# Optimization experiments

Hardware: AMD Instinct MI355X
Metric: run time of the kernel (lower is better)

The kernel has to match this reference:

```python
import jax, jax.numpy as jnp
import numpy as np

EPS = 1e-8  # torch cosine_similarity eps


def setup_inputs() -> dict:
    key = jax.random.key(0)
    ks = jax.random.split(key, 6)
    N, D, E, mask_dim = 50000, 128, 600000, 1
    x = jax.random.normal(ks[0], (N, D), dtype=jnp.float32)
    mask = jax.random.normal(ks[1], (N, mask_dim), dtype=jnp.float32)
    edge_index = jax.random.randint(ks[2], (2, E), 0, N, dtype=jnp.int64)
    # Linear(input_dim, input_dim) params (orthogonal-ish init not needed for math check)
    W = jax.random.normal(ks[3], (D, D), dtype=jnp.float32) / np.sqrt(D)
    b_lin = jax.random.normal(ks[4], (D,), dtype=jnp.float32) * 0.01
    alpha = jnp.float32(0.001)
    bias = jnp.ones((mask_dim,), dtype=jnp.float32) * -3.0
    return {"x": x, "mask": mask, "edge_index": edge_index,
            "W": W, "b_lin": b_lin, "alpha": alpha, "bias": bias}


def _forward(x, mask, W, b_lin, alpha, bias, edge_index, K=5):
    N = x.shape[0]
    # x_fn: Linear + Tanh
    h = jnp.tanh(x @ W.T + b_lin)                    # [N, D]
    row, col = edge_index[0], edge_index[1]
    hs, hd = h[row], h[col]                          # [E, D] gathers
    ns = jnp.maximum(jnp.linalg.norm(hs, axis=-1), EPS)
    nd = jnp.maximum(jnp.linalg.norm(hd, axis=-1), EPS)
    cos = jnp.sum(hs * hd, axis=-1) / (ns * nd)      # [E]
    edge_weights = jax.nn.relu(cos)

    # APPNP with PyG defaults: gcn_norm with self-loops (weight 1), sym norm
    loops = jnp.arange(N, dtype=row.dtype)
    r2 = jnp.concatenate([row, loops])
    c2 = jnp.concatenate([col, loops])
    w2 = jnp.concatenate([edge_weights, jnp.ones((N,), dtype=edge_weights.dtype)])
    deg = jax.ops.segment_sum(w2, c2, num_segments=N)
    dinv = jnp.where(deg > 0, deg ** -0.5, 0.0)
    norm = dinv[r2] * w2 * dinv[c2]                  # [E+N]

    h0 = jax.nn.relu(mask)                           # [N, 1]
    f = h0
    for _ in range(K):
        msg = norm[:, None] * f[r2]                  # gather + weight
        agg = jax.ops.segment_sum(msg, c2, num_segments=N)  # scatter-add to targets
        f = (1.0 - alpha) * agg + alpha * h0
    fill = jnp.tanh(f - jax.nn.softplus(bias))
    return fill, edge_weights


def reference(x, mask, edge_index, W, b_lin, alpha, bias):
    return _forward(x, mask, W, b_lin, alpha, bias, edge_index, K=5)
```

## Files before the change

### kernel.cpp

```cpp
#include <hip/hip_runtime.h>
#include <hip/hip_bf16.h>
#include <hip/hip_fp16.h>
#include <math.h>

typedef _Float16 half8 __attribute__((ext_vector_type(8)));
typedef float f32x4 __attribute__((ext_vector_type(4)));

__device__ __forceinline__ float tanh_fast(float v) {
  float e = __expf(v + v);
  return 1.0f - 2.0f * __builtin_amdgcn_rcpf(e + 1.0f);
}

__device__ __forceinline__ float dot8h(float4 a, float4 b) {
  const __half2* pa = (const __half2*)&a;
  const __half2* pb = (const __half2*)&b;
  float s = 0.0f;
#pragma unroll
  for (int i = 0; i < 4; ++i) {
    float2 fa = __half22float2(pa[i]);
    float2 fb = __half22float2(pb[i]);
    s = fmaf(fa.x, fb.x, s);
    s = fmaf(fa.y, fb.y, s);
  }
  return s;
}

__global__ __launch_bounds__(256) void k_front(
    const float* __restrict__ x, const float* __restrict__ W,
    const float* __restrict__ bl, const float* __restrict__ mask,
    const int* __restrict__ cols, __half* __restrict__ hn,
    int* __restrict__ cnt, float* __restrict__ h0, float* __restrict__ f_a,
    int N, int E, int nblk) {
  __shared__ _Float16 wsh[128 * 128];
  const int tid = threadIdx.x;
  const int bid = blockIdx.x;
  const int NTILES = (N + 63) / 64;

  if (bid < NTILES) {
    for (int i = tid; i < 2048; i += 256) {
      int row = i >> 4, cc = i & 15;
      const float4* wr = (const float4*)(W + row * 128 + cc * 8);
      float4 a = wr[0], b = wr[1];
      half8 h;
      h[0] = (_Float16)a.x; h[1] = (_Float16)a.y;
      h[2] = (_Float16)a.z; h[3] = (_Float16)a.w;
      h[4] = (_Float16)b.x; h[5] = (_Float16)b.y;
      h[6] = (_Float16)b.z; h[7] = (_Float16)b.w;
      *(half8*)((char*)wsh + row * 256 + ((cc * 16) ^ ((row & 7) << 4))) = h;
    }
    __syncthreads();

    const int wv = tid >> 6, lane = tid & 63;
    const int row0 = bid * 64 + wv * 16;
    if (row0 < N) {
      const int r = lane & 15;
      const int g = lane >> 4;
      half8 afrag[4];
      {
        const float4* xr = (const float4*)(x + (size_t)(row0 + r) * 128);
#pragma unroll
        for (int ks = 0; ks < 4; ++ks) {
          float4 lo = xr[ks * 8 + g * 2];
          float4 hi = xr[ks * 8 + g * 2 + 1];
          half8 a;
          a[0] = (_Float16)lo.x; a[1] = (_Float16)lo.y;
          a[2] = (_Float16)lo.z; a[3] = (_Float16)lo.w;
          a[4] = (_Float16)hi.x; a[5] = (_Float16)hi.y;
          a[6] = (_Float16)hi.z; a[7] = (_Float16)hi.w;
          afrag[ks] = a;
        }
      }
      f32x4 acc[8];
#pragma unroll
      for (int c = 0; c < 8; ++c) acc[c] = (f32x4){0.f, 0.f, 0.f, 0.f};
#pragma unroll
      for (int c = 0; c < 8; ++c) {
        const char* base = (const char*)wsh + (c * 16 + r) * 256;
        const int sw = ((c * 16 + r) & 7) << 4;
#pragma unroll
        for (int ks = 0; ks < 4; ++ks) {
          half8 b = *(const half8*)(base + ((ks * 64 + g * 16) ^ sw));
          acc[c] = __builtin_amdgcn_mfma_f32_16x16x32_f16(afrag[ks], b,
                                                          acc[c], 0, 0, 0);
        }
      }
      float t[8][4];
      float ss[4] = {0.f, 0.f, 0.f, 0.f};
#pragma unroll
      for (int c = 0; c < 8; ++c) {
        float bv = bl[c * 16 + r];
#pragma unroll
        for (int j = 0; j < 4; ++j) {
          float tv = tanh_fast(acc[c][j] + bv);
          t[c][j] = tv;
          ss[j] = fmaf(tv, tv, ss[j]);
        }
      }
#pragma unroll
      for (int j = 0; j < 4; ++j) {
#pragma unroll
        for (int o = 8; o; o >>= 1) ss[j] += __shfl_xor(ss[j], o);
        ss[j] = 1.0f / fmaxf(sqrtf(ss[j]), 1e-8f);
      }
#pragma unroll
      for (int c = 0; c < 8; ++c)
#pragma unroll
        for (int j = 0; j < 4; ++j)
          hn[(size_t)(row0 + g * 4 + j) * 128 + c * 16 + r] =
              __float2half_rn(t[c][j] * ss[j]);
    }
  }

  const int tg = bid * 256 + tid;
  const int NT = nblk * 256;
  for (int i = tg; i < N; i += NT) {
    float v = fmaxf(mask[i], 0.0f);
    h0[i] = v;
    f_a[i] = v;
  }
  for (int e = tg; e < E; e += NT) atomicAdd(cnt + cols[e], 1);
}

__global__ __launch_bounds__(256) void k_scan_a(const int* __restrict__ cnt,
                                                int* __restrict__ bsum,
                                                int N) {
  __shared__ int s[256];
  int i = blockIdx.x * 256 + threadIdx.x;
  s[threadIdx.x] = (i < N) ? cnt[i] : 0;
  __syncthreads();
  for (int d = 128; d; d >>= 1) {
    if (threadIdx.x < d) s[threadIdx.x] += s[threadIdx.x + d];
    __syncthreads();
  }
  if (threadIdx.x == 0) bsum[blockIdx.x] = s[0];
}

__global__ __launch_bounds__(256) void k_scan_bc(
    const int* __restrict__ cnt, const int* __restrict__ bsum,
    int* __restrict__ off, int* __restrict__ cursor, int N, int E, int NCH) {
  __shared__ int bscan[2 * 256];
  __shared__ int cscan[2 * 256];
  const int t = threadIdx.x, bid = blockIdx.x;
  int bv = (t < NCH) ? bsum[t] : 0;
  bscan[t] = bv;
  __syncthreads();
  int a = 0;
  for (int d = 1; d < 256; d <<= 1) {
    int v2 = bscan[a * 256 + t];
    if (t >= d) v2 += bscan[a * 256 + t - d];
    bscan[(a ^ 1) * 256 + t] = v2;
    __syncthreads();
    a ^= 1;
  }
  int bpre = (bid > 0) ? bscan[a * 256 + bid - 1] : 0;
  int i = bid * 256 + t;
  int v = (i < N) ? cnt[i] : 0;
  cscan[t] = v;
  __syncthreads();
  int b2 = 0;
  for (int d = 1; d < 256; d <<= 1) {
    int v2 = cscan[b2 * 256 + t];
    if (t >= d) v2 += cscan[b2 * 256 + t - d];
    cscan[(b2 ^ 1) * 256 + t] = v2;
    __syncthreads();
    b2 ^= 1;
  }
  int excl = cscan[b2 * 256 + t] - v + bpre;
  if (i < N) {
    off[i] = excl;
    cursor[i] = excl;
  }
  if (i == 0) off[N] = E;
}

__global__ void k_build(const int* __restrict__ rows,
                        const int* __restrict__ cols, int* __restrict__ cursor,
                        unsigned* __restrict__ rec, int* __restrict__ perm,
                        int E) {
  int e = blockIdx.x * 256 + threadIdx.x;
  if (e >= E) return;
  unsigned r = (unsigned)rows[e], c = (unsigned)cols[e];
  int pos = atomicAdd(cursor + c, 1);
  rec[pos] = r | (c << 16);
  perm[e] = pos;
}

__global__ __launch_bounds__(256) void k_edge_cos(
    const __half* __restrict__ hn, const unsigned* __restrict__ rec,
    float* __restrict__ csr_w, unsigned short* __restrict__ src16, int E,
    int Q) {
  int t = blockIdx.x * 256 + threadIdx.x;
  int q = t >> 2, sub = t & 3;
  if (q >= Q) return;
  const int p0 = q, p1 = q + Q;
  const bool has1 = p1 < E;
  unsigned rc0 = rec[p0];
  unsigned rc1 = has1 ? rec[p1] : rc0;
  const float4* hr0 = (const float4*)(hn + (size_t)(rc0 & 0xffffu) * 128);
  const float4* hr1 = (const float4*)(hn + (size_t)(rc1 & 0xffffu) * 128);
  float4 r00 = hr0[sub], r01 = hr0[sub + 4], r02 = hr0[sub + 8],
         r03 = hr0[sub + 12];
  float4 r10 = hr1[sub], r11 = hr1[sub + 4], r12 = hr1[sub + 8],
         r13 = hr1[sub + 12];
  const float4* hc0 = (const float4*)(hn + (size_t)(rc0 >> 16) * 128);
  const float4* hc1 = (const float4*)(hn + (size_t)(rc1 >> 16) * 128);
  float d0 = dot8h(r00, hc0[sub]) + dot8h(r01, hc0[sub + 4]) +
             dot8h(r02, hc0[sub + 8]) + dot8h(r03, hc0[sub + 12]);
  float d1 = dot8h(r10, hc1[sub]) + dot8h(r11, hc1[sub + 4]) +
             dot8h(r12, hc1[sub + 8]) + dot8h(r13, hc1[sub + 12]);
  d0 += __shfl_xor(d0, 1);
  d0 += __shfl_xor(d0, 2);
  d1 += __shfl_xor(d1, 1);
  d1 += __shfl_xor(d1, 2);
  if (sub == 0) {
    csr_w[p0] = fmaxf(d0, 0.0f);
    src16[p0] = (unsigned short)(rc0 & 0xffffu);
    if (has1) {
      csr_w[p1] = fmaxf(d1, 0.0f);
      src16[p1] = (unsigned short)(rc1 & 0xffffu);
    }
  }
}

__global__ __launch_bounds__(256) void k_unperm_rsd(
    const float* __restrict__ csr_w, const int* __restrict__ perm,
    const int* __restrict__ off, float* __restrict__ ew,
    float* __restrict__ rsd, int N, int E) {
  int t = blockIdx.x * 256 + threadIdx.x;
  if (t < E) ew[t] = csr_w[perm[t]];
  int n = t >> 2, sub = t & 3;
  if (n < N) {
    int s0 = off[n], s1 = off[n + 1];
    float s = 0.0f;
    for (int i = s0 + sub; i < s1; i += 4) s += csr_w[i];
    s += __shfl_xor(s, 1);
    s += __shfl_xor(s, 2);
    if (sub == 0) rsd[n] = rsqrtf(1.0f + s);
  }
}

__global__ __launch_bounds__(256) void k_prop(
    const float* __restrict__ f_in, float* __restrict__ f_out,
    float* __restrict__ csr_w, const unsigned short* __restrict__ src16,
    const int* __restrict__ off, const float* __restrict__ h0,
    const float* __restrict__ rsd, const float* __restrict__ alpha_p,
    const float* __restrict__ bias_p, float* __restrict__ fill, int N,
    int mode) {
  int t = blockIdx.x * 256 + threadIdx.x;
  int n = t >> 2, sub = t & 3;
  if (n >= N) return;
  float rs_n = rsd[n];
  int s0 = off[n], s1 = off[n + 1];
  float part = 0.0f;
  if (mode & 1) {
    for (int i = s0 + sub; i < s1; i += 4) {
      int s = src16[i];
      float wn = csr_w[i] * rs_n * rsd[s];
      csr_w[i] = wn;
      part = fmaf(wn, f_in[s], part);
    }
  } else {
    for (int i = s0 + sub; i < s1; i += 4)
      part = fmaf(csr_w[i], f_in[src16[i]], part);
  }
  part += __shfl_xor(part, 1);
  part += __shfl_xor(part, 2);
  if (sub == 0) {
    float a = alpha_p[0];
    float agg = part + f_in[n] * rs_n * rs_n;
    float fn = (1.0f - a) * agg + a * h0[n];
    if (mode & 2) {
      float b = bias_p[0];
      float sp = (b > 20.0f) ? b : log1pf(expf(b));
      fill[n] = tanhf(fn - sp);
    } else {
      f_out[n] = fn;
    }
  }
}

extern "C" void kernel_launch(void* const* d_in, const int* in_sizes, int n_in,
                              void* d_out, int out_size, void* d_ws,
                              size_t ws_size, hipStream_t stream) {
  const float* x = (const float*)d_in[0];
  const float* mask = (const float*)d_in[1];
  const int* ei = (const int*)d_in[2];
  const float* W = (const float*)d_in[3];
  const float* bl = (const float*)d_in[4];
  const float* alpha = (const float*)d_in[5];
  const float* bias = (const float*)d_in[6];

  const int D = 128;
  const int N = in_sizes[0] / D;
  const int E = in_sizes[2] / 2;
  const int* rows = ei;
  const int* cols = ei + E;

  float* fill = (float*)d_out;
  float* ew = (float*)d_out + N;

  char* w = (char*)d_ws;
  size_t off_b = 0;
  auto alloc = [&](size_t bytes) -> void* {
    void* p = (void*)(w + off_b);
    off_b = (off_b + bytes + 255) & ~(size_t)255;
    return p;
  };
  __half* hn = (__half*)alloc((size_t)N * D * sizeof(__half));
  int* cnt = (int*)alloc((size_t)N * sizeof(int));
  int* off = (int*)alloc((size_t)(N + 1) * sizeof(int));
  int* cursor = (int*)alloc((size_t)N * sizeof(int));
  int* bsum = (int*)alloc(256 * sizeof(int));
  unsigned* rec = (unsigned*)alloc((size_t)E * sizeof(unsigned));
  int* perm = (int*)alloc((size_t)E * sizeof(int));
  float* csr_w = (float*)alloc((size_t)E * sizeof(float));
  unsigned short* src16 =
      (unsigned short*)alloc((size_t)E * sizeof(unsigned short));
  float* h0 = (float*)alloc((size_t)N * sizeof(float));
  float* f_a = (float*)alloc((size_t)N * sizeof(float));
  float* f_b = (float*)alloc((size_t)N * sizeof(float));
  float* rsd = (float*)alloc((size_t)N * sizeof(float));
  (void)ws_size;

  const int NCH = (N + 255) / 256;
  const int nb_E = (E + 255) / 256;
  const int FRONT_BLOCKS = 1024;

  hipMemsetAsync(cnt, 0, (size_t)N * sizeof(int), stream);
  k_front<<<FRONT_BLOCKS, 256, 0, stream>>>(x, W, bl, mask, cols, hn, cnt, h0,
                                            f_a, N, E, FRONT_BLOCKS);
  k_scan_a<<<NCH, 256, 0, stream>>>(cnt, bsum, N);
  k_scan_bc<<<NCH, 256, 0, stream>>>(cnt, bsum, off, cursor, N, E, NCH);
  k_build<<<nb_E, 256, 0, stream>>>(rows, cols, cursor, rec, perm, E);
  const int Q = (E + 1) / 2;
  k_edge_cos<<<(Q * 4 + 255) / 256, 256, 0, stream>>>(hn, rec, csr_w, src16,
                                                      E, Q);
  k_unperm_rsd<<<nb_E, 256, 0, stream>>>(csr_w, perm, off, ew, rsd, N, E);
  const float* fi = f_a;
  float* fo = f_b;
  for (int it = 0; it < 5; ++it) {
    int mode = (it == 0 ? 1 : 0) | (it == 4 ? 2 : 0);
    k_prop<<<(N * 4 + 255) / 256, 256, 0, stream>>>(
        fi, fo, csr_w, src16, off, h0, rsd, alpha, bias, fill, N, mode);
    const float* tmp = fo;
    fo = (float*)fi;
    fi = tmp;
  }
}
```

Measured before the change: 143.3 us.

## Pre-convert W to fp16 once and load MFMA B fragments from global memory

A small kernel now converts W to fp16 once. k_front drops its per-block shared-memory staging of W and the block barrier, and instead loads the B fragments straight from global memory (cache-resident) into registers, in two halves. This removes 64KB of LDS per block and the repeated fp32-to-fp16 conversion in each block, which should raise occupancy. The cost is more register pressure, one extra launch, and a front grid sized to N/64 blocks instead of 1024, which changes how the grid-stride mask and degree-count loops spread their work.

```diff
diff --git a/kernel.cpp b/kernel.cpp
--- a/kernel.cpp
+++ b/kernel.cpp
@@ -25,90 +25,99 @@
   return s;
 }
 
+__global__ void k_conv_w(const float* __restrict__ W,
+                         _Float16* __restrict__ Wh) {
+  int i = blockIdx.x * 256 + threadIdx.x;
+  float4 v = ((const float4*)W)[i];
+  _Float16 o[4] = {(_Float16)v.x, (_Float16)v.y, (_Float16)v.z, (_Float16)v.w};
+  *(short4*)((short*)Wh + i * 4) = *(short4*)o;
+}
+
 __global__ __launch_bounds__(256) void k_front(
-    const float* __restrict__ x, const float* __restrict__ W,
+    const float* __restrict__ x, const _Float16* __restrict__ Wh,
     const float* __restrict__ bl, const float* __restrict__ mask,
     const int* __restrict__ cols, __half* __restrict__ hn,
     int* __restrict__ cnt, float* __restrict__ h0, float* __restrict__ f_a,
     int N, int E, int nblk) {
-  __shared__ _Float16 wsh[128 * 128];
-  const int tid = threadIdx.x;
-  const int bid = blockIdx.x;
-  const int NTILES = (N + 63) / 64;
-
-  if (bid < NTILES) {
-    for (int i = tid; i < 2048; i += 256) {
-      int row = i >> 4, cc = i & 15;
-      const float4* wr = (const float4*)(W + row * 128 + cc * 8);
-      float4 a = wr[0], b = wr[1];
-      half8 h;
-      h[0] = (_Float16)a.x; h[1] = (_Float16)a.y;
-      h[2] = (_Float16)a.z; h[3] = (_Float16)a.w;
-      h[4] = (_Float16)b.x; h[5] = (_Float16)b.y;
-      h[6] = (_Float16)b.z; h[7] = (_Float16)b.w;
-      *(half8*)((char*)wsh + row * 256 + ((cc * 16) ^ ((row & 7) << 4))) = h;
-    }
-    __syncthreads();
-
-    const int wv = tid >> 6, lane = tid & 63;
-    const int row0 = bid * 64 + wv * 16;
-    if (row0 < N) {
-      const int r = lane & 15;
-      const int g = lane >> 4;
-      half8 afrag[4];
-      {
-        const float4* xr = (const float4*)(x + (size_t)(row0 + r) * 128);
-#pragma unroll
-        for (int ks = 0; ks < 4; ++ks) {
-          float4 lo = xr[ks * 8 + g * 2];
-          float4 hi = xr[ks * 8 + g * 2 + 1];
-          half8 a;
-          a[0] = (_Float16)lo.x; a[1] = (_Float16)lo.y;
-          a[2] = (_Float16)lo.z; a[3] = (_Float16)lo.w;
-          a[4] = (_Float16)hi.x; a[5] = (_Float16)hi.y;
-          a[6] = (_Float16)hi.z; a[7] = (_Float16)hi.w;
-          afrag[ks] = a;
-        }
+  const int tid = threadIdx.x, bid = blockIdx.x;
+  const int wv = tid >> 6, lane = tid & 63;
+  const int row0 = (bid * 4 + wv) * 16;
+  const int r = lane & 15;
+  const int g = lane >> 4;
+
+  if (row0 < N) {
+    float4 xv[8];
+    const float4* xr = (const float4*)(x + (size_t)(row0 + r) * 128);
+#pragma unroll
+    for (int ks = 0; ks < 4; ++ks) {
+      xv[ks * 2] = xr[ks * 8 + g * 2];
+      xv[ks * 2 + 1] = xr[ks * 8 + g * 2 + 1];
+    }
+    half8 bfr[16];
+#pragma unroll
+    for (int c = 0; c < 4; ++c)
+#pragma unroll
+      for (int ks = 0; ks < 4; ++ks)
+        bfr[c * 4 + ks] =
+            *(const half8*)(Wh + (size_t)(c * 16 + r) * 128 + ks * 32 + g * 8);
+    half8 afrag[4];
+#pragma unroll
+    for (int ks = 0; ks < 4; ++ks) {
+      float4 lo = xv[ks * 2], hi = xv[ks * 2 + 1];
+      half8 a;
+      a[0] = (_Float16)lo.x; a[1] = (_Float16)lo.y;
+      a[2] = (_Float16)lo.z; a[3] = (_Float16)lo.w;
+      a[4] = (_Float16)hi.x; a[5] = (_Float16)hi.y;
+      a[6] = (_Float16)hi.z; a[7] = (_Float16)hi.w;
+      afrag[ks] = a;
+    }
+    f32x4 acc[8];
+#pragma unroll
+    for (int c = 0; c < 8; ++c) acc[c] = (f32x4){0.f, 0.f, 0.f, 0.f};
+#pragma unroll
+    for (int c = 0; c < 4; ++c)
+#pragma unroll
+      for (int ks = 0; ks < 4; ++ks)
+        acc[c] = __builtin_amdgcn_mfma_f32_16x16x32_f16(afrag[ks],
+                                                        bfr[c * 4 + ks],
+                                                        acc[c], 0, 0, 0);
+#pragma unroll
+    for (int c = 4; c < 8; ++c)
+#pragma unroll
+      for (int ks = 0; ks < 4; ++ks)
+        bfr[(c - 4) * 4 + ks] =
+            *(const half8*)(Wh + (size_t)(c * 16 + r) * 128 + ks * 32 + g * 8);
+#pragma unroll
+    for (int c = 4; c < 8; ++c)
+#pragma unroll
+      for (int ks = 0; ks < 4; ++ks)
+        acc[c] = __builtin_amdgcn_mfma_f32_16x16x32_f16(afrag[ks],
+                                                        bfr[(c - 4) * 4 + ks],
+                                                        acc[c], 0, 0, 0);
+    float t[8][4];
+    float ss[4] = {0.f, 0.f, 0.f, 0.f};
+#pragma unroll
+    for (int c = 0; c < 8; ++c) {
+      float bv = bl[c * 16 + r];
+#pragma unroll
+      for (int j = 0; j < 4; ++j) {
+        float tv = tanh_fast(acc[c][j] + bv);
+        t[c][j] = tv;
+        ss[j] = fmaf(tv, tv, ss[j]);
       }
-      f32x4 acc[8];
-#pragma unroll
-      for (int c = 0; c < 8; ++c) acc[c] = (f32x4){0.f, 0.f, 0.f, 0.f};
-#pragma unroll
-      for (int c = 0; c < 8; ++c) {
-        const char* base = (const char*)wsh + (c * 16 + r) * 256;
-        const int sw = ((c * 16 + r) & 7) << 4;
-#pragma unroll
-        for (int ks = 0; ks < 4; ++ks) {
-          half8 b = *(const half8*)(base + ((ks * 64 + g * 16) ^ sw));
-          acc[c] = __builtin_amdgcn_mfma_f32_16x16x32_f16(afrag[ks], b,
-                                                          acc[c], 0, 0, 0);
-        }
-      }
-      float t[8][4];
-      float ss[4] = {0.f, 0.f, 0.f, 0.f};
-#pragma unroll
-      for (int c = 0; c < 8; ++c) {
-        float bv = bl[c * 16 + r];
-#pragma unroll
-        for (int j = 0; j < 4; ++j) {
-          float tv = tanh_fast(acc[c][j] + bv);
-          t[c][j] = tv;
-          ss[j] = fmaf(tv, tv, ss[j]);
-        }
-      }
-#pragma unroll
-      for (int j = 0; j < 4; ++j) {
-#pragma unroll
-        for (int o = 8; o; o >>= 1) ss[j] += __shfl_xor(ss[j], o);
-        ss[j] = 1.0f / fmaxf(sqrtf(ss[j]), 1e-8f);
-      }
-#pragma unroll
-      for (int c = 0; c < 8; ++c)
-#pragma unroll
-        for (int j = 0; j < 4; ++j)
-          hn[(size_t)(row0 + g * 4 + j) * 128 + c * 16 + r] =
-              __float2half_rn(t[c][j] * ss[j]);
-    }
+    }
+#pragma unroll
+    for (int j = 0; j < 4; ++j) {
+#pragma unroll
+      for (int o = 8; o; o >>= 1) ss[j] += __shfl_xor(ss[j], o);
+      ss[j] = 1.0f / fmaxf(sqrtf(ss[j]), 1e-8f);
+    }
+#pragma unroll
+    for (int c = 0; c < 8; ++c)
+#pragma unroll
+      for (int j = 0; j < 4; ++j)
+        hn[(size_t)(row0 + g * 4 + j) * 128 + c * 16 + r] =
+            __float2half_rn(t[c][j] * ss[j]);
   }
 
   const int tg = bid * 256 + tid;
@@ -307,6 +316,7 @@
     return p;
   };
   __half* hn = (__half*)alloc((size_t)N * D * sizeof(__half));
+  _Float16* Wh = (_Float16*)alloc((size_t)D * D * sizeof(_Float16));
   int* cnt = (int*)alloc((size_t)N * sizeof(int));
   int* off = (int*)alloc((size_t)(N + 1) * sizeof(int));
   int* cursor = (int*)alloc((size_t)N * sizeof(int));
@@ -324,11 +334,12 @@
 
   const int NCH = (N + 255) / 256;
   const int nb_E = (E + 255) / 256;
-  const int FRONT_BLOCKS = 1024;
+  const int FRONT_BLOCKS = (N + 63) / 64;
 
   hipMemsetAsync(cnt, 0, (size_t)N * sizeof(int), stream);
-  k_front<<<FRONT_BLOCKS, 256, 0, stream>>>(x, W, bl, mask, cols, hn, cnt, h0,
-                                            f_a, N, E, FRONT_BLOCKS);
+  k_conv_w<<<16, 256, 0, stream>>>(W, Wh);
+  k_front<<<FRONT_BLOCKS, 256, 0, stream>>>(x, Wh, bl, mask, cols, hn, cnt,
+                                            h0, f_a, N, E, FRONT_BLOCKS);
   k_scan_a<<<NCH, 256, 0, stream>>>(cnt, bsum, N);
   k_scan_bc<<<NCH, 256, 0, stream>>>(cnt, bsum, off, cursor, N, E, NCH);
   k_build<<<nb_E, 256, 0, stream>>>(rows, cols, cursor, rec, perm, E);
```

Result: slower. 155.8 us (+8.8%).

## Record per-edge rank in 8 privatized counters to remove build-phase atomics

Applied to the files above, without the earlier changes.

The degree histogram is split into 8 privatized copies chosen by edge block, and each edge stores its atomicAdd return value as a 16-bit rank. The scan then turns the per-copy counts into per-copy base offsets, so the CSR build computes each edge's position without a second round of atomics on a cursor array. The front kernel's grid is also changed to exactly N/64 blocks, with every block doing the GEMM tile. This costs a larger memset and counter array plus an extra rank buffer, and it assumes per-copy counts fit in 16 bits.

```diff
diff --git a/kernel.cpp b/kernel.cpp
--- a/kernel.cpp
+++ b/kernel.cpp
@@ -29,86 +29,83 @@
     const float* __restrict__ x, const float* __restrict__ W,
     const float* __restrict__ bl, const float* __restrict__ mask,
     const int* __restrict__ cols, __half* __restrict__ hn,
-    int* __restrict__ cnt, float* __restrict__ h0, float* __restrict__ f_a,
-    int N, int E, int nblk) {
+    int* __restrict__ cnt8, unsigned short* __restrict__ rank,
+    float* __restrict__ h0, float* __restrict__ f_a, int N, int E, int nblk) {
   __shared__ _Float16 wsh[128 * 128];
   const int tid = threadIdx.x;
   const int bid = blockIdx.x;
-  const int NTILES = (N + 63) / 64;
-
-  if (bid < NTILES) {
-    for (int i = tid; i < 2048; i += 256) {
-      int row = i >> 4, cc = i & 15;
-      const float4* wr = (const float4*)(W + row * 128 + cc * 8);
-      float4 a = wr[0], b = wr[1];
-      half8 h;
-      h[0] = (_Float16)a.x; h[1] = (_Float16)a.y;
-      h[2] = (_Float16)a.z; h[3] = (_Float16)a.w;
-      h[4] = (_Float16)b.x; h[5] = (_Float16)b.y;
-      h[6] = (_Float16)b.z; h[7] = (_Float16)b.w;
-      *(half8*)((char*)wsh + row * 256 + ((cc * 16) ^ ((row & 7) << 4))) = h;
-    }
-    __syncthreads();
-
-    const int wv = tid >> 6, lane = tid & 63;
-    const int row0 = bid * 64 + wv * 16;
-    if (row0 < N) {
-      const int r = lane & 15;
-      const int g = lane >> 4;
-      half8 afrag[4];
-      {
-        const float4* xr = (const float4*)(x + (size_t)(row0 + r) * 128);
-#pragma unroll
-        for (int ks = 0; ks < 4; ++ks) {
-          float4 lo = xr[ks * 8 + g * 2];
-          float4 hi = xr[ks * 8 + g * 2 + 1];
-          half8 a;
-          a[0] = (_Float16)lo.x; a[1] = (_Float16)lo.y;
-          a[2] = (_Float16)lo.z; a[3] = (_Float16)lo.w;
-          a[4] = (_Float16)hi.x; a[5] = (_Float16)hi.y;
-          a[6] = (_Float16)hi.z; a[7] = (_Float16)hi.w;
-          afrag[ks] = a;
-        }
+
+  for (int i = tid; i < 2048; i += 256) {
+    int row = i >> 4, cc = i & 15;
+    const float4* wr = (const float4*)(W + row * 128 + cc * 8);
+    float4 a = wr[0], b = wr[1];
+    half8 h;
+    h[0] = (_Float16)a.x; h[1] = (_Float16)a.y;
+    h[2] = (_Float16)a.z; h[3] = (_Float16)a.w;
+    h[4] = (_Float16)b.x; h[5] = (_Float16)b.y;
+    h[6] = (_Float16)b.z; h[7] = (_Float16)b.w;
+    *(half8*)((char*)wsh + row * 256 + ((cc * 16) ^ ((row & 7) << 4))) = h;
+  }
+  __syncthreads();
+
+  const int wv = tid >> 6, lane = tid & 63;
+  const int row0 = bid * 64 + wv * 16;
+  if (row0 < N) {
+    const int r = lane & 15;
+    const int g = lane >> 4;
+    half8 afrag[4];
+    {
+      const float4* xr = (const float4*)(x + (size_t)(row0 + r) * 128);
+#pragma unroll
+      for (int ks = 0; ks < 4; ++ks) {
+        float4 lo = xr[ks * 8 + g * 2];
+        float4 hi = xr[ks * 8 + g * 2 + 1];
+        half8 a;
+        a[0] = (_Float16)lo.x; a[1] = (_Float16)lo.y;
+        a[2] = (_Float16)lo.z; a[3] = (_Float16)lo.w;
+        a[4] = (_Float16)hi.x; a[5] = (_Float16)hi.y;
+        a[6] = (_Float16)hi.z; a[7] = (_Float16)hi.w;
+        afrag[ks] = a;
       }
-      f32x4 acc[8];
-#pragma unroll
-      for (int c = 0; c < 8; ++c) acc[c] = (f32x4){0.f, 0.f, 0.f, 0.f};
-#pragma unroll
-      for (int c = 0; c < 8; ++c) {
-        const char* base = (const char*)wsh + (c * 16 + r) * 256;
-        const int sw = ((c * 16 + r) & 7) << 4;
-#pragma unroll
-        for (int ks = 0; ks < 4; ++ks) {
-          half8 b = *(const half8*)(base + ((ks * 64 + g * 16) ^ sw));
-          acc[c] = __builtin_amdgcn_mfma_f32_16x16x32_f16(afrag[ks], b,
-                                                          acc[c], 0, 0, 0);
-        }
+    }
+    f32x4 acc[8];
+#pragma unroll
+    for (int c = 0; c < 8; ++c) acc[c] = (f32x4){0.f, 0.f, 0.f, 0.f};
+#pragma unroll
+    for (int c = 0; c < 8; ++c) {
+      const char* base = (const char*)wsh + (c * 16 + r) * 256;
+      const int sw = ((c * 16 + r) & 7) << 4;
+#pragma unroll
+      for (int ks = 0; ks < 4; ++ks) {
+        half8 b = *(const half8*)(base + ((ks * 64 + g * 16) ^ sw));
+        acc[c] = __builtin_amdgcn_mfma_f32_16x16x32_f16(afrag[ks], b, acc[c],
+                                                        0, 0, 0);
       }
-      float t[8][4];
-      float ss[4] = {0.f, 0.f, 0.f, 0.f};
-#pragma unroll
-      for (int c = 0; c < 8; ++c) {
-        float bv = bl[c * 16 + r];
-#pragma unroll
-        for (int j = 0; j < 4; ++j) {
-          float tv = tanh_fast(acc[c][j] + bv);
-          t[c][j] = tv;
-          ss[j] = fmaf(tv, tv, ss[j]);
-        }
+    }
+    float t[8][4];
+    float ss[4] = {0.f, 0.f, 0.f, 0.f};
+#pragma unroll
+    for (int c = 0; c < 8; ++c) {
+      float bv = bl[c * 16 + r];
+#pragma unroll
+      for (int j = 0; j < 4; ++j) {
+        float tv = tanh_fast(acc[c][j] + bv);
+        t[c][j] = tv;
+        ss[j] = fmaf(tv, tv, ss[j]);
       }
-#pragma unroll
-      for (int j = 0; j < 4; ++j) {
-#pragma unroll
-        for (int o = 8; o; o >>= 1) ss[j] += __shfl_xor(ss[j], o);
-        ss[j] = 1.0f / fmaxf(sqrtf(ss[j]), 1e-8f);
-      }
-#pragma unroll
-      for (int c = 0; c < 8; ++c)
-#pragma unroll
-        for (int j = 0; j < 4; ++j)
-          hn[(size_t)(row0 + g * 4 + j) * 128 + c * 16 + r] =
-              __float2half_rn(t[c][j] * ss[j]);
-    }
+    }
+#pragma unroll
+    for (int j = 0; j < 4; ++j) {
+#pragma unroll
+      for (int o = 8; o; o >>= 1) ss[j] += __shfl_xor(ss[j], o);
+      ss[j] = 1.0f / fmaxf(sqrtf(ss[j]), 1e-8f);
+    }
+#pragma unroll
+    for (int c = 0; c < 8; ++c)
+#pragma unroll
+      for (int j = 0; j < 4; ++j)
+        hn[(size_t)(row0 + g * 4 + j) * 128 + c * 16 + r] =
+            __float2half_rn(t[c][j] * ss[j]);
   }
 
   const int tg = bid * 256 + tid;
@@ -118,15 +115,25 @@
     h0[i] = v;
     f_a[i] = v;
   }
-  for (int e = tg; e < E; e += NT) atomicAdd(cnt + cols[e], 1);
-}
-
-__global__ __launch_bounds__(256) void k_scan_a(const int* __restrict__ cnt,
+  for (int e = tg; e < E; e += NT) {
+    int c = cols[e];
+    int copy = (e >> 8) & 7;
+    int rk = atomicAdd(cnt8 + copy * N + c, 1);
+    rank[e] = (unsigned short)rk;
+  }
+}
+
+__global__ __launch_bounds__(256) void k_scan_a(const int* __restrict__ cnt8,
                                                 int* __restrict__ bsum,
                                                 int N) {
   __shared__ int s[256];
   int i = blockIdx.x * 256 + threadIdx.x;
-  s[threadIdx.x] = (i < N) ? cnt[i] : 0;
+  int tot = 0;
+  if (i < N) {
+#pragma unroll
+    for (int j = 0; j < 8; ++j) tot += cnt8[j * N + i];
+  }
+  s[threadIdx.x] = tot;
   __syncthreads();
   for (int d = 128; d; d >>= 1) {
     if (threadIdx.x < d) s[threadIdx.x] += s[threadIdx.x + d];
@@ -135,9 +142,10 @@
   if (threadIdx.x == 0) bsum[blockIdx.x] = s[0];
 }
 
-__global__ __launch_bounds__(256) void k_scan_bc(
-    const int* __restrict__ cnt, const int* __restrict__ bsum,
-    int* __restrict__ off, int* __restrict__ cursor, int N, int E, int NCH) {
+__global__ __launch_bounds__(256) void k_scan_bc(int* __restrict__ cnt8,
+                                                 const int* __restrict__ bsum,
+                                                 int* __restrict__ off, int N,
+                                                 int E, int NCH) {
   __shared__ int bscan[2 * 256];
   __shared__ int cscan[2 * 256];
   const int t = threadIdx.x, bid = blockIdx.x;
@@ -154,8 +162,16 @@
   }
   int bpre = (bid > 0) ? bscan[a * 256 + bid - 1] : 0;
   int i = bid * 256 + t;
-  int v = (i < N) ? cnt[i] : 0;
-  cscan[t] = v;
+  int cj[8];
+  int tot = 0;
+  if (i < N) {
+#pragma unroll
+    for (int j = 0; j < 8; ++j) {
+      cj[j] = cnt8[j * N + i];
+      tot += cj[j];
+    }
+  }
+  cscan[t] = tot;
   __syncthreads();
   int b2 = 0;
   for (int d = 1; d < 256; d <<= 1) {
@@ -165,22 +181,30 @@
     __syncthreads();
     b2 ^= 1;
   }
-  int excl = cscan[b2 * 256 + t] - v + bpre;
   if (i < N) {
+    int excl = cscan[b2 * 256 + t] - tot + bpre;
     off[i] = excl;
-    cursor[i] = excl;
-  }
-  if (i == 0) off[N] = E;
+    int run = excl;
+#pragma unroll
+    for (int j = 0; j < 8; ++j) {
+      cnt8[j * N + i] = run;
+      run += cj[j];
+    }
+  }
+  if (bid == 0 && t == 0) off[N] = E;
 }
 
 __global__ void k_build(const int* __restrict__ rows,
-                        const int* __restrict__ cols, int* __restrict__ cursor,
+                        const int* __restrict__ cols,
+                        const int* __restrict__ base8,
+                        const unsigned short* __restrict__ rank,
                         unsigned* __restrict__ rec, int* __restrict__ perm,
-                        int E) {
+                        int N, int E) {
   int e = blockIdx.x * 256 + threadIdx.x;
   if (e >= E) return;
   unsigned r = (unsigned)rows[e], c = (unsigned)cols[e];
-  int pos = atomicAdd(cursor + c, 1);
+  int copy = (e >> 8) & 7;
+  int pos = base8[copy * N + (int)c] + (int)rank[e];
   rec[pos] = r | (c << 16);
   perm[e] = pos;
 }
@@ -307,9 +331,10 @@
     return p;
   };
   __half* hn = (__half*)alloc((size_t)N * D * sizeof(__half));
-  int* cnt = (int*)alloc((size_t)N * sizeof(int));
+  int* cnt8 = (int*)alloc((size_t)8 * N * sizeof(int));
+  unsigned short* rank =
+      (unsigned short*)alloc((size_t)E * sizeof(unsigned short));
   int* off = (int*)alloc((size_t)(N + 1) * sizeof(int));
-  int* cursor = (int*)alloc((size_t)N * sizeof(int));
   int* bsum = (int*)alloc(256 * sizeof(int));
   unsigned* rec = (unsigned*)alloc((size_t)E * sizeof(unsigned));
   int* perm = (int*)alloc((size_t)E * sizeof(int));
@@ -324,14 +349,14 @@
 
   const int NCH = (N + 255) / 256;
   const int nb_E = (E + 255) / 256;
-  const int FRONT_BLOCKS = 1024;
-
-  hipMemsetAsync(cnt, 0, (size_t)N * sizeof(int), stream);
-  k_front<<<FRONT_BLOCKS, 256, 0, stream>>>(x, W, bl, mask, cols, hn, cnt, h0,
-                                            f_a, N, E, FRONT_BLOCKS);
-  k_scan_a<<<NCH, 256, 0, stream>>>(cnt, bsum, N);
-  k_scan_bc<<<NCH, 256, 0, stream>>>(cnt, bsum, off, cursor, N, E, NCH);
-  k_build<<<nb_E, 256, 0, stream>>>(rows, cols, cursor, rec, perm, E);
+  const int FRONT_BLOCKS = (N + 63) / 64;
+
+  hipMemsetAsync(cnt8, 0, (size_t)8 * N * sizeof(int), stream);
+  k_front<<<FRONT_BLOCKS, 256, 0, stream>>>(x, W, bl, mask, cols, hn, cnt8,
+                                            rank, h0, f_a, N, E, FRONT_BLOCKS);
+  k_scan_a<<<NCH, 256, 0, stream>>>(cnt8, bsum, N);
+  k_scan_bc<<<NCH, 256, 0, stream>>>(cnt8, bsum, off, N, E, NCH);
+  k_build<<<nb_E, 256, 0, stream>>>(rows, cols, cnt8, rank, rec, perm, N, E);
   const int Q = (E + 1) / 2;
   k_edge_cos<<<(Q * 4 + 255) / 256, 256, 0, stream>>>(hn, rec, csr_w, src16,
                                                       E, Q);
```

Result: faster. 120.6 us (-15.8%).
